# Kernel optimization log

Measured on AMD Instinct MI355X. Metric: run time of the kernel, lower is better.

## Reference

```python
import jax, jax.numpy as jnp
import numpy as np

# 7 axial hex directions (dy, dx) including center, matching HexConv2d.DIRS
DIRS = [(0, 0), (1, 0), (0, 1), (-1, 1), (-1, 0), (0, -1), (1, -1)]


def _shift(x, dy, dx):
    """torch.roll-style shift with zero fill at wrapped edges. x: [B,C,H,W]."""
    sx, sy = -dx, -dy
    y = jnp.roll(x, shift=(sy, sx), axis=(2, 3))
    if sy > 0:
        y = y.at[:, :, :sy, :].set(0)
    elif sy < 0:
        y = y.at[:, :, sy:, :].set(0)
    if sx > 0:
        y = y.at[:, :, :, :sx].set(0)
    elif sx < 0:
        y = y.at[:, :, :, sx:].set(0)
    return y


def _hex_mask(H, dtype):
    size = H // 2
    q = jnp.arange(-size, size + 1)
    Q, R = jnp.meshgrid(q, q, indexing='ij')
    S = -Q - R
    # |Q|<=size and |R|<=size hold by construction; only |S|<=size cuts corners
    mask = ((jnp.abs(Q) <= size) & (jnp.abs(R) <= size) & (jnp.abs(S) <= size))
    return mask.astype(dtype)[None, None]  # [1,1,H,W]


def setup_inputs() -> dict:
    key = jax.random.key(0)
    k1, k2, k3 = jax.random.split(key, 3)
    B, Cin, Cout, H = 32, 256, 256, 49
    x = jax.random.normal(k1, (B, Cin, H, H), dtype=jnp.float32)
    weight = jax.random.normal(k2, (Cout, Cin, 7), dtype=jnp.float32) * 0.02
    bias = jax.random.normal(k3, (Cout,), dtype=jnp.float32) * 0.02
    return {"x": x, "weight": weight, "bias": bias}


def reference(x, weight, bias):
    mask = _hex_mask(x.shape[2], x.dtype)          # [1,1,H,W]
    x = x * mask
    # [7,B,C,H,W]: shifted+masked neighbor maps
    nbr = jnp.stack([_shift(x, dy, dx) for (dy, dx) in DIRS], axis=0) * mask
    # fused 1x1 conv over (channel, direction): weight [O,C,7]
    y = jnp.einsum('nbchw,ocn->bohw', nbr, weight) + bias[None, :, None, None]
    return y * mask
```

## Files before the change

### kernel.cpp

```cpp
#include <hip/hip_runtime.h>


typedef __attribute__((ext_vector_type(8))) short short8;
typedef __attribute__((ext_vector_type(4))) short short4v;
typedef __attribute__((ext_vector_type(4))) float floatx4;

#define NPIX   2401
#define W50    50
#define PREAL  2450
#define XBLEAD 56
#define XBROWS 2672
#define NT4    39
#define NSEG4  11
#define BUFB4  (NSEG4*1024)
#define XB3_BYTES ((size_t)32*XBROWS*256*2)
#define WP_BYTES  917504ULL
#define WS_NEED3  (XB3_BYTES + WP_BYTES)

__device__ __forceinline__ unsigned short f2bf(float f) {
  unsigned u = __builtin_bit_cast(unsigned, f);
  u += 0x7fffu + ((u >> 16) & 1u);
  return (unsigned short)(u >> 16);
}

__global__ void prep_w_kernel(const float* __restrict__ w, unsigned short* __restrict__ wp) {
  int t = blockIdx.x * 256 + threadIdx.x;
  int l  = t & 63;
  int ot = (t >> 6) & 15;
  int kc = (t >> 10) & 7;
  int n  = t >> 13;
  int o  = ot * 16 + (l & 15);
  int cb = kc * 32 + ((l >> 4) * 8);
  const float* src = w + (size_t)(o * 256 + cb) * 7 + n;
  short8 pk;
#pragma unroll
  for (int j = 0; j < 8; ++j) pk[j] = (short)f2bf(src[j * 7]);
  ((short8*)wp)[t] = pk;
}

__global__ void zero_pads(unsigned short* __restrict__ xb) {
  int idx = blockIdx.x * 256 + threadIdx.x;
  int c16 = idx & 31;
  int rb  = idx >> 5;
  int row = rb % XBROWS;
  int b   = rb / XBROWS;
  int p   = row - XBLEAD;
  bool pad = (p < 0) || (p >= PREAL) || (p % W50 == 49);
  if (pad) {
    short8 z = {0,0,0,0,0,0,0,0};
    *(short8*)(xb + ((size_t)b * XBROWS + row) * 256 + c16 * 8) = z;
  }
}

__global__ __launch_bounds__(256)
void prep_x4(const float* __restrict__ x, unsigned short* __restrict__ xb) {
  __shared__ unsigned short t[64][68];
  const int tid = threadIdx.x;
  const int span = blockIdx.x, cg = blockIdx.y, b = blockIdx.z;
  const int s0 = span * 64;
  {
    const int chl = tid >> 2, i4 = tid & 3;
    const float* src = x + ((size_t)(b * 256 + cg * 64 + chl)) * NPIX;
    const int rbase = s0 + i4 * 16;
#pragma unroll
    for (int it = 0; it < 4; ++it) {
      int r = rbase + it * 4;
      float vv[4] = {0.f, 0.f, 0.f, 0.f};
      if (r + 3 < NPIX) {
        float4 v = *(const float4*)(src + r);
        vv[0] = v.x; vv[1] = v.y; vv[2] = v.z; vv[3] = v.w;
      } else {
#pragma unroll
        for (int e = 0; e < 4; ++e) if (r + e < NPIX) vv[e] = src[r + e];
      }
      short4v u = {0, 0, 0, 0};
#pragma unroll
      for (int e = 0; e < 4; ++e) {
        int re = r + e;
        unsigned short uu = 0;
        if (re < NPIX) {
          int h = re / 49, w = re - h * 49, s = h + w;
          if (s >= 24 && s <= 72) uu = f2bf(vv[e]);
        }
        u[e] = (short)uu;
      }
      *(short4v*)&t[chl][i4 * 16 + it * 4] = u;
    }
  }
  __syncthreads();
  const int pp = tid >> 3;
  const int co = tid & 7;
  unsigned d[8];
#pragma unroll
  for (int k = 0; k < 8; ++k) d[k] = *(const unsigned*)&t[co * 8 + k][pp * 2];
  uint4 lo, hi;
  {
    unsigned l0[4], h0[4];
#pragma unroll
    for (int m = 0; m < 4; ++m) {
      unsigned a = d[2 * m], bq = d[2 * m + 1];
      l0[m] = (a & 0xffffu) | (bq << 16);
      h0[m] = (a >> 16) | (bq & 0xffff0000u);
    }
    lo = make_uint4(l0[0], l0[1], l0[2], l0[3]);
    hi = make_uint4(h0[0], h0[1], h0[2], h0[3]);
  }
  const int r_lo = s0 + pp * 2, r_hi = r_lo + 1;
  if (r_lo < NPIX) {
    int prow = r_lo + r_lo / 49 + XBLEAD;
    *(uint4*)(xb + ((size_t)b * XBROWS + prow) * 256 + cg * 64 + co * 8) = lo;
  }
  if (r_hi < NPIX) {
    int prow = r_hi + r_hi / 49 + XBLEAD;
    *(uint4*)(xb + ((size_t)b * XBROWS + prow) * 256 + cg * 64 + co * 8) = hi;
  }
}

__global__ __launch_bounds__(256, 3)
void hexconv_v4(const unsigned short* __restrict__ xb,
                const unsigned short* __restrict__ wp,
                const float* __restrict__ bias,
                float* __restrict__ out) {
  __shared__ __attribute__((aligned(16))) unsigned char smem[2 * BUFB4];

  const int tid  = threadIdx.x;
  const int lane = tid & 63;
  const int wv   = tid >> 6;
  const int col  = lane & 15;
  const int quad = lane >> 4;

  const int pt = blockIdx.x;
  const int b  = blockIdx.y;
  const int P0 = pt * 64;
  const int phase = (pt + b * 3) & 7;

  const int OFF[7] = {0, 50, 1, -49, -50, -1, 49};

  int ba[7];
#pragma unroll
  for (int n = 0; n < 7; ++n) {
    int r0 = col + 56 + OFF[n];
    int r64 = r0 << 6;
    ba[n] = (r64 + quad * 16) ^ ((r64 >> 3) & 0x30);
  }

  const int gpart = (lane & 3) ^ ((lane >> 3) & 3);
  const char* gsrc0 = (const char*)(xb + ((size_t)b * XBROWS + (size_t)P0) * 256)
                      + (lane >> 2) * 512 + gpart * 16;

  auto stage = [&](int buf, int kc) {
    char* ldsb = (char*)smem + buf * BUFB4;
    for (int s = wv; s < NSEG4; s += 4)
      __builtin_amdgcn_global_load_lds(
          (const __attribute__((address_space(1))) unsigned int*)(gsrc0 + (size_t)s * 8192 + kc * 64),
          (__attribute__((address_space(3))) unsigned int*)(ldsb + s * 1024), 16, 0, 0);
  };

  const char* wbase = (const char*)wp + (size_t)(wv * 4) * 1024 + lane * 16;

  floatx4 acc[4][4];
#pragma unroll
  for (int ii = 0; ii < 4; ++ii)
#pragma unroll
    for (int j = 0; j < 4; ++j) acc[ii][j] = (floatx4){0.f, 0.f, 0.f, 0.f};

  stage(0, phase);
  __syncthreads();

  for (int i = 0; i < 8; ++i) {
    const int kc  = (i + phase) & 7;
    const int kcn = (i + 1 + phase) & 7;
    if (i < 7) stage((i + 1) & 1, kcn);
    const char* bufp = (const char*)smem + (i & 1) * BUFB4;
#pragma unroll
    for (int n = 0; n < 7; ++n) {
      short8 af[4];
#pragma unroll
      for (int ii = 0; ii < 4; ++ii)
        af[ii] = *(const short8*)(wbase + ((size_t)((n * 8 + kc) * 16 + ii)) * 1024);
      short8 bf[4];
#pragma unroll
      for (int j = 0; j < 4; ++j)
        bf[j] = *(const short8*)(bufp + ba[n] + j * 1024);
#pragma unroll
      for (int ii = 0; ii < 4; ++ii)
#pragma unroll
        for (int j = 0; j < 4; ++j)
          acc[ii][j] = __builtin_amdgcn_mfma_f32_16x16x32_bf16(af[ii], bf[j], acc[ii][j], 0, 0, 0);
    }
    __syncthreads();
  }

  const int ob = wv * 64;
  floatx4 bv[4];
#pragma unroll
  for (int ii = 0; ii < 4; ++ii)
    bv[ii] = *(const floatx4*)(bias + ob + ii * 16 + quad * 4);

#pragma unroll
  for (int j = 0; j < 4; ++j) {
    int p = P0 + j * 16 + col;
    int h = p / W50;
    int w = p - h * W50;
    if (w >= 49 || p >= PREAL) continue;
    bool m = (h + w >= 24) && (h + w <= 72);
    size_t ridx = (size_t)h * 49 + w;
#pragma unroll
    for (int ii = 0; ii < 4; ++ii) {
      float* dst = out + ((size_t)(b * 256 + ob + ii * 16 + quad * 4)) * NPIX + ridx;
#pragma unroll
      for (int rr = 0; rr < 4; ++rr) {
        float v = m ? (acc[ii][j][rr] + bv[ii][rr]) : 0.f;
        dst[(size_t)rr * NPIX] = v;
      }
    }
  }
}

#define PITCH  40
#define V1WIN  168
#define V1ZROW 168
__global__ __launch_bounds__(256)
void hexconv_v1(const float* __restrict__ x,
                const unsigned short* __restrict__ wp,
                const float* __restrict__ bias,
                float* __restrict__ out) {
  __shared__ unsigned short sm[(V1ZROW + 2) * PITCH];
  const int tid = threadIdx.x, lane = tid & 63, wv = tid >> 6;
  const int col = lane & 15, quad = lane >> 4;
  const int pt = blockIdx.x, b = blockIdx.y;
  const int P0 = pt * 64, win_start = P0 - 52;
  if (tid < PITCH * 2) sm[V1ZROW * PITCH + tid] = 0;
  const int OFF[7] = {0, 49, 1, -48, -49, -1, 48};
  const int DXP = (1 << 2) | (1 << 3), DXN = (1 << 5) | (1 << 6);
  int baddr[4][7];
#pragma unroll
  for (int j = 0; j < 4; ++j) {
    int pix = P0 + j * 16 + col;
    int wj = pix % 49;
    int rowbase = pix - win_start;
#pragma unroll
    for (int n = 0; n < 7; ++n) {
      bool bad = (((DXP >> n) & 1) && wj == 48) || (((DXN >> n) & 1) && wj == 0);
      int row = bad ? V1ZROW : (rowbase + OFF[n]);
      baddr[j][n] = row * (PITCH * 2) + quad * 16;
    }
  }
  int sp[3], sgp[3]; bool sok[3];
#pragma unroll
  for (int pi = 0; pi < 3; ++pi) {
    int p = lane + pi * 64, gp = win_start + p;
    sp[pi] = p; sgp[pi] = gp;
    bool hm = false;
    if (gp >= 0 && gp < NPIX) { int h = gp / 49, w = gp - h * 49, s = h + w; hm = (s >= 24 && s <= 72); }
    sok[pi] = (p < V1WIN) && hm;
  }
  floatx4 acc[4][4];
#pragma unroll
  for (int i = 0; i < 4; ++i)
#pragma unroll
    for (int j = 0; j < 4; ++j) acc[i][j] = (floatx4){0.f, 0.f, 0.f, 0.f};
  const short8* wpv = (const short8*)wp;
  const int wslot = wv * 4;
  for (int kc = 0; kc < 8; ++kc) {
    __syncthreads();
#pragma unroll
    for (int ci = 0; ci < 8; ++ci) {
      int c = ci * 4 + wv;
      const float* src = x + ((size_t)(b * 256 + kc * 32 + c)) * NPIX;
#pragma unroll
      for (int pi = 0; pi < 3; ++pi) {
        if (sp[pi] < V1WIN) {
          float v = sok[pi] ? src[sgp[pi]] : 0.f;
          sm[sp[pi] * PITCH + c] = f2bf(v);
        }
      }
    }
    __syncthreads();
#pragma unroll
    for (int n = 0; n < 7; ++n) {
      short8 af[4];
#pragma unroll
      for (int i = 0; i < 4; ++i)
        af[i] = wpv[((size_t)((n * 8 + kc) * 16 + wslot + i)) * 64 + lane];
      short8 bf[4];
#pragma unroll
      for (int j = 0; j < 4; ++j)
        bf[j] = *(const short8*)((const char*)sm + baddr[j][n]);
#pragma unroll
      for (int i = 0; i < 4; ++i)
#pragma unroll
        for (int j = 0; j < 4; ++j)
          acc[i][j] = __builtin_amdgcn_mfma_f32_16x16x32_bf16(af[i], bf[j], acc[i][j], 0, 0, 0);
    }
  }
  const int ob = wv * 64;
  floatx4 bv[4];
#pragma unroll
  for (int i = 0; i < 4; ++i)
    bv[i] = *(const floatx4*)(bias + ob + i * 16 + quad * 4);
#pragma unroll
  for (int j = 0; j < 4; ++j) {
    int pix = P0 + j * 16 + col;
    if (pix >= NPIX) continue;
    int h = pix / 49, w = pix - h * 49;
    bool m = (h + w >= 24 && h + w <= 72);
#pragma unroll
    for (int i = 0; i < 4; ++i) {
      int o = ob + i * 16 + quad * 4;
      float* dst = out + ((size_t)(b * 256 + o)) * NPIX + pix;
#pragma unroll
      for (int r = 0; r < 4; ++r) {
        float v = m ? (acc[i][j][r] + bv[i][r]) : 0.f;
        dst[(size_t)r * NPIX] = v;
      }
    }
  }
}

extern "C" void kernel_launch(void* const* d_in, const int* in_sizes, int n_in,
                              void* d_out, int out_size, void* d_ws, size_t ws_size,
                              hipStream_t stream) {
  const float* x    = (const float*)d_in[0];
  const float* w    = (const float*)d_in[1];
  const float* bias = (const float*)d_in[2];
  float* out = (float*)d_out;

  if (ws_size >= WS_NEED3) {
    unsigned short* xb = (unsigned short*)d_ws;
    unsigned short* wp = (unsigned short*)((char*)d_ws + XB3_BYTES);
    zero_pads<<<(32 * XBROWS * 32) / 256, 256, 0, stream>>>(xb);
    prep_w_kernel<<<224, 256, 0, stream>>>(w, wp);
    prep_x4<<<dim3(38, 4, 32), 256, 0, stream>>>(x, xb);
    hexconv_v4<<<dim3(NT4, 32), 256, 0, stream>>>(xb, wp, bias, out);
  } else {
    unsigned short* wp = (unsigned short*)d_ws;
    prep_w_kernel<<<224, 256, 0, stream>>>(w, wp);
    hexconv_v1<<<dim3(38, 32), 256, 0, stream>>>(x, wp, bias, out);
  }
}
```

Measured before the change: 265.0 us.

## Widen hex conv pixel tile to 128 and stage two K chunks per step

The main conv kernel now covers 128 pixels per block instead of 64, so each weight fragment loaded feeds 8 MFMA column tiles rather than 4. Each pipeline step stages two K chunks at once, halving the number of barriers and main-loop iterations. The pad-zeroing kernel now visits only the pad rows instead of scanning every row. In exchange the accumulator count and LDS use double, occupancy drops to 2 blocks per CU, and the grid shrinks to 640 blocks, which may underfill the GPU.

```diff
diff --git a/kernel.cpp b/kernel.cpp
--- a/kernel.cpp
+++ b/kernel.cpp
@@ -10,12 +10,14 @@
 #define PREAL  2450
 #define XBLEAD 56
 #define XBROWS 2672
-#define NT4    39
-#define NSEG4  11
-#define BUFB4  (NSEG4*1024)
+#define PT5    128
+#define NT5    20
+#define NSEG5  15
+#define BUF5   (2*NSEG5*1024)
 #define XB3_BYTES ((size_t)32*XBROWS*256*2)
 #define WP_BYTES  917504ULL
 #define WS_NEED3  (XB3_BYTES + WP_BYTES)
+#define NPADROW 271
 
 __device__ __forceinline__ unsigned short f2bf(float f) {
   unsigned u = __builtin_bit_cast(unsigned, f);
@@ -38,18 +40,19 @@
   ((short8*)wp)[t] = pk;
 }
 
-__global__ void zero_pads(unsigned short* __restrict__ xb) {
+__global__ void zero_pads5(unsigned short* __restrict__ xb) {
   int idx = blockIdx.x * 256 + threadIdx.x;
+  if (idx >= 32 * NPADROW * 32) return;
   int c16 = idx & 31;
-  int rb  = idx >> 5;
-  int row = rb % XBROWS;
-  int b   = rb / XBROWS;
-  int p   = row - XBLEAD;
-  bool pad = (p < 0) || (p >= PREAL) || (p % W50 == 49);
-  if (pad) {
-    short8 z = {0,0,0,0,0,0,0,0};
-    *(short8*)(xb + ((size_t)b * XBROWS + row) * 256 + c16 * 8) = z;
-  }
+  int rr  = idx >> 5;
+  int pr  = rr % NPADROW;
+  int b   = rr / NPADROW;
+  int row;
+  if (pr < 56)        row = pr;
+  else if (pr < 105)  row = 105 + 50 * (pr - 56);
+  else                row = 2506 + (pr - 105);
+  short8 z = {0,0,0,0,0,0,0,0};
+  *(short8*)(xb + ((size_t)b * XBROWS + row) * 256 + c16 * 8) = z;
 }
 
 __global__ __launch_bounds__(256)
@@ -116,12 +119,12 @@
   }
 }
 
-__global__ __launch_bounds__(256, 3)
-void hexconv_v4(const unsigned short* __restrict__ xb,
+__global__ __launch_bounds__(256, 2)
+void hexconv_v5(const unsigned short* __restrict__ xb,
                 const unsigned short* __restrict__ wp,
                 const float* __restrict__ bias,
                 float* __restrict__ out) {
-  __shared__ __attribute__((aligned(16))) unsigned char smem[2 * BUFB4];
+  __shared__ __attribute__((aligned(16))) unsigned char smem[2 * BUF5];
 
   const int tid  = threadIdx.x;
   const int lane = tid & 63;
@@ -131,8 +134,8 @@
 
   const int pt = blockIdx.x;
   const int b  = blockIdx.y;
-  const int P0 = pt * 64;
-  const int phase = (pt + b * 3) & 7;
+  const int P0 = pt * PT5;
+  const int phase = ((pt + b) & 3) * 2;
 
   const int OFF[7] = {0, 50, 1, -49, -50, -1, 49};
 
@@ -148,45 +151,54 @@
   const char* gsrc0 = (const char*)(xb + ((size_t)b * XBROWS + (size_t)P0) * 256)
                       + (lane >> 2) * 512 + gpart * 16;
 
-  auto stage = [&](int buf, int kc) {
-    char* ldsb = (char*)smem + buf * BUFB4;
-    for (int s = wv; s < NSEG4; s += 4)
+  auto stage2 = [&](int buf, int kc0) {
+    char* ldsb = (char*)smem + buf * BUF5;
+    for (int u = wv; u < 2 * NSEG5; u += 4) {
+      int kk = (u >= NSEG5) ? 1 : 0;
+      int s  = u - kk * NSEG5;
       __builtin_amdgcn_global_load_lds(
-          (const __attribute__((address_space(1))) unsigned int*)(gsrc0 + (size_t)s * 8192 + kc * 64),
-          (__attribute__((address_space(3))) unsigned int*)(ldsb + s * 1024), 16, 0, 0);
+          (const __attribute__((address_space(1))) unsigned int*)
+              (gsrc0 + (size_t)s * 8192 + (kc0 + kk) * 64),
+          (__attribute__((address_space(3))) unsigned int*)(ldsb + u * 1024), 16, 0, 0);
+    }
   };
 
   const char* wbase = (const char*)wp + (size_t)(wv * 4) * 1024 + lane * 16;
 
-  floatx4 acc[4][4];
+  floatx4 acc[4][8];
 #pragma unroll
   for (int ii = 0; ii < 4; ++ii)
 #pragma unroll
-    for (int j = 0; j < 4; ++j) acc[ii][j] = (floatx4){0.f, 0.f, 0.f, 0.f};
-
-  stage(0, phase);
+    for (int j = 0; j < 8; ++j) acc[ii][j] = (floatx4){0.f, 0.f, 0.f, 0.f};
+
+  stage2(0, phase);
   __syncthreads();
 
-  for (int i = 0; i < 8; ++i) {
-    const int kc  = (i + phase) & 7;
-    const int kcn = (i + 1 + phase) & 7;
-    if (i < 7) stage((i + 1) & 1, kcn);
-    const char* bufp = (const char*)smem + (i & 1) * BUFB4;
+  for (int i = 0; i < 4; ++i) {
+    const int kc0  = (2 * i + phase) & 7;
+    const int kc0n = (2 * i + 2 + phase) & 7;
+    if (i < 3) stage2((i + 1) & 1, kc0n);
+    const char* bufp = (const char*)smem + (i & 1) * BUF5;
 #pragma unroll
     for (int n = 0; n < 7; ++n) {
-      short8 af[4];
-#pragma unroll
-      for (int ii = 0; ii < 4; ++ii)
-        af[ii] = *(const short8*)(wbase + ((size_t)((n * 8 + kc) * 16 + ii)) * 1024);
-      short8 bf[4];
-#pragma unroll
-      for (int j = 0; j < 4; ++j)
-        bf[j] = *(const short8*)(bufp + ba[n] + j * 1024);
-#pragma unroll
-      for (int ii = 0; ii < 4; ++ii)
-#pragma unroll
-        for (int j = 0; j < 4; ++j)
-          acc[ii][j] = __builtin_amdgcn_mfma_f32_16x16x32_bf16(af[ii], bf[j], acc[ii][j], 0, 0, 0);
+#pragma unroll
+      for (int kk = 0; kk < 2; ++kk) {
+        const int kc = kc0 + kk;
+        short8 af[4];
+#pragma unroll
+        for (int ii = 0; ii < 4; ++ii)
+          af[ii] = *(const short8*)(wbase + ((size_t)((n * 8 + kc) * 16 + ii)) * 1024);
+        const char* bp = bufp + kk * (NSEG5 * 1024) + ba[n];
+        short8 bf[8];
+#pragma unroll
+        for (int j = 0; j < 8; ++j)
+          bf[j] = *(const short8*)(bp + j * 1024);
+#pragma unroll
+        for (int ii = 0; ii < 4; ++ii)
+#pragma unroll
+          for (int j = 0; j < 8; ++j)
+            acc[ii][j] = __builtin_amdgcn_mfma_f32_16x16x32_bf16(af[ii], bf[j], acc[ii][j], 0, 0, 0);
+      }
     }
     __syncthreads();
   }
@@ -198,7 +210,7 @@
     bv[ii] = *(const floatx4*)(bias + ob + ii * 16 + quad * 4);
 
 #pragma unroll
-  for (int j = 0; j < 4; ++j) {
+  for (int j = 0; j < 8; ++j) {
     int p = P0 + j * 16 + col;
     int h = p / W50;
     int w = p - h * W50;
@@ -329,10 +341,10 @@
   if (ws_size >= WS_NEED3) {
     unsigned short* xb = (unsigned short*)d_ws;
     unsigned short* wp = (unsigned short*)((char*)d_ws + XB3_BYTES);
-    zero_pads<<<(32 * XBROWS * 32) / 256, 256, 0, stream>>>(xb);
+    zero_pads5<<<(32 * NPADROW * 32 + 255) / 256, 256, 0, stream>>>(xb);
     prep_w_kernel<<<224, 256, 0, stream>>>(w, wp);
     prep_x4<<<dim3(38, 4, 32), 256, 0, stream>>>(x, xb);
-    hexconv_v4<<<dim3(NT4, 32), 256, 0, stream>>>(xb, wp, bias, out);
+    hexconv_v5<<<dim3(NT5, 32), 256, 0, stream>>>(xb, wp, bias, out);
   } else {
     unsigned short* wp = (unsigned short*)d_ws;
     prep_w_kernel<<<224, 256, 0, stream>>>(w, wp);
```

Result: faster. 244.2 us (-7.8%).
